# Performance work log

Hardware: AMD Instinct MI355X
Metric: run time of the kernel (lower is better)

Reference implementation:

```python
import jax, jax.numpy as jnp
import numpy as np

B, S, D, H = 2, 2048, 1024, 16
DH = D // H
EPS = 1e-5
NEG = -1e9


def layer_norm(x, scale, bias):
    mu = jnp.mean(x, axis=-1, keepdims=True)
    var = jnp.mean((x - mu) ** 2, axis=-1, keepdims=True)
    return (x - mu) * jax.lax.rsqrt(var + EPS) * scale + bias


def setup_inputs() -> dict:
    key = jax.random.key(0)
    ks = jax.random.split(key, 8)
    scale = 1.0 / np.sqrt(D)
    x = jax.random.normal(ks[0], (B, S, D), dtype=jnp.float32)
    padding_mask = jnp.ones((B, S), dtype=bool)
    # per-head QKV projections stacked over heads: (H, D, DH)
    Wq = jax.random.normal(ks[1], (H, D, DH), dtype=jnp.float32) * scale
    Wk = jax.random.normal(ks[2], (H, D, DH), dtype=jnp.float32) * scale
    Wv = jax.random.normal(ks[3], (H, D, DH), dtype=jnp.float32) * scale
    ln1_s = jnp.ones((D,), jnp.float32); ln1_b = jnp.zeros((D,), jnp.float32)
    ln2_s = jnp.ones((D,), jnp.float32); ln2_b = jnp.zeros((D,), jnp.float32)
    W1 = jax.random.normal(ks[4], (D, D), dtype=jnp.float32) * scale
    b1 = jnp.zeros((D,), jnp.float32)
    W2 = jax.random.normal(ks[5], (D, D), dtype=jnp.float32) * scale
    b2 = jnp.zeros((D,), jnp.float32)
    return dict(x=x, padding_mask=padding_mask, Wq=Wq, Wk=Wk, Wv=Wv,
                ln1_s=ln1_s, ln1_b=ln1_b, ln2_s=ln2_s, ln2_b=ln2_b,
                W1=W1, b1=b1, W2=W2, b2=b2)


def reference(x, padding_mask, Wq, Wk, Wv, ln1_s, ln1_b, ln2_s, ln2_b, W1, b1, W2, b2):
    # pre-norm attention with residual (dropout = identity at eval)
    h = layer_norm(x, ln1_s, ln1_b)
    q = jnp.einsum('bsd,hde->bhse', h, Wq)
    k = jnp.einsum('bsd,hde->bhse', h, Wk)
    v = jnp.einsum('bsd,hde->bhse', h, Wv)
    scores = jnp.einsum('bhse,bhte->bhst', q, k) / jnp.sqrt(jnp.float32(DH))
    causal = jnp.tril(jnp.ones((S, S), dtype=bool))           # (S,S)
    mask = padding_mask[:, None, None, :] & causal[None, None]  # (B,1,S,S)
    scores = jnp.where(mask, scores, NEG)
    p = jax.nn.softmax(scores, axis=-1)
    z = jnp.einsum('bhst,bhte->bshe', p, v).reshape(x.shape[0], x.shape[1], D)
    x = x + z
    # pre-norm FFN with residual
    h2 = layer_norm(x, ln2_s, ln2_b)
    ff = jax.nn.relu(h2 @ W1 + b1) @ W2 + b2
    return x + ff
```

## Files before the change

kernel.cpp:

```cpp
#include <hip/hip_runtime.h>
#include <hip/hip_bf16.h>
#include <stdint.h>

#define NB 2
#define NS 2048
#define ND 1024
#define NH 16
#define NDH 64
#define NT (NB*NS)

using f32x4  = __attribute__((ext_vector_type(4))) float;
using bf16x8 = __attribute__((ext_vector_type(8))) short;

typedef __attribute__((address_space(1))) unsigned int as1_uint;
typedef __attribute__((address_space(3))) unsigned int as3_uint;

#if __has_builtin(__builtin_amdgcn_exp2f)
#define EXP2 __builtin_amdgcn_exp2f
#else
#define EXP2 exp2f
#endif

__device__ __forceinline__ void llds16(void* l, const void* g) {
    __builtin_amdgcn_global_load_lds((as1_uint*)g, (as3_uint*)l, 16, 0, 0);
}

__device__ __forceinline__ f32x4 mfma16(bf16x8 a, bf16x8 b, f32x4 c) {
    return __builtin_amdgcn_mfma_f32_16x16x32_bf16(a, b, c, 0, 0, 0);
}

__device__ __forceinline__ unsigned short f2bf(float f) {
    union { __hip_bfloat16 h; unsigned short u; } cv;
    cv.h = __float2bfloat16(f);
    return cv.u;
}

__global__ void k_prep_ln(const float* __restrict__ Wq, const float* __restrict__ Wk,
                          const float* __restrict__ Wv, const float* __restrict__ W1,
                          const float* __restrict__ W2, unsigned short* __restrict__ WcatT,
                          unsigned short* __restrict__ W1T, unsigned short* __restrict__ W2T,
                          const float* __restrict__ x, const float* __restrict__ sc,
                          const float* __restrict__ bi, unsigned short* __restrict__ hout) {
    __shared__ float tile[64][65];
    __shared__ float ssum[4], ssq[4];
    int tid = threadIdx.x;
    int bid = blockIdx.x;
    if (bid < 768) {
        const float SCALEQ = 0.125f * 1.44269504088896f;
        int kt = bid & 15; bid >>= 4;
        int h  = bid & 15; bid >>= 4;
        int mat = bid;
        const float* W = (mat == 0) ? Wq : (mat == 1) ? Wk : Wv;
#pragma unroll
        for (int i = 0; i < 16; ++i) {
            int idx = tid + i * 256;
            int r = idx >> 6, e = idx & 63;
            tile[r][e] = W[(size_t)h * ND * NDH + (size_t)(kt * 64 + r) * NDH + e];
        }
        __syncthreads();
#pragma unroll
        for (int i = 0; i < 16; ++i) {
            int idx = tid + i * 256;
            int e = idx >> 6, r = idx & 63;
            float v = tile[r][e];
            if (mat == 0) v *= SCALEQ;
            WcatT[(size_t)(mat * 1024 + h * 64 + e) * ND + kt * 64 + r] = f2bf(v);
        }
    } else if (bid < 1280) {
        const float* W = (bid < 1024) ? W1 : W2;
        unsigned short* WT = (bid < 1024) ? W1T : W2T;
        int lb = (bid - 768) & 255;
        int ntile = lb & 15;
        int ktile = lb >> 4;
#pragma unroll
        for (int i = 0; i < 16; ++i) {
            int idx = tid + i * 256;
            int r = idx >> 6, c = idx & 63;
            tile[r][c] = W[(size_t)(ktile * 64 + r) * ND + ntile * 64 + c];
        }
        __syncthreads();
#pragma unroll
        for (int i = 0; i < 16; ++i) {
            int idx = tid + i * 256;
            int c = idx >> 6, r = idx & 63;
            WT[(size_t)(ntile * 64 + c) * ND + ktile * 64 + r] = f2bf(tile[r][c]);
        }
    } else {
        int row = bid - 1280;
        const float* xr = x + (size_t)row * ND;
        float4 v = reinterpret_cast<const float4*>(xr)[tid];
        float sum = v.x + v.y + v.z + v.w;
        float sq  = v.x * v.x + v.y * v.y + v.z * v.z + v.w * v.w;
#pragma unroll
        for (int off = 1; off < 64; off <<= 1) {
            sum += __shfl_xor(sum, off);
            sq  += __shfl_xor(sq, off);
        }
        int wave = tid >> 6;
        if ((tid & 63) == 0) { ssum[wave] = sum; ssq[wave] = sq; }
        __syncthreads();
        sum = ssum[0] + ssum[1] + ssum[2] + ssum[3];
        sq  = ssq[0] + ssq[1] + ssq[2] + ssq[3];
        float mu  = sum * (1.0f / ND);
        float var = sq * (1.0f / ND) - mu * mu;
        float rstd = rsqrtf(var + 1e-5f);
        float4 s4 = reinterpret_cast<const float4*>(sc)[tid];
        float4 b4 = reinterpret_cast<const float4*>(bi)[tid];
        ushort4 o;
        o.x = f2bf((v.x - mu) * rstd * s4.x + b4.x);
        o.y = f2bf((v.y - mu) * rstd * s4.y + b4.y);
        o.z = f2bf((v.z - mu) * rstd * s4.z + b4.z);
        o.w = f2bf((v.w - mu) * rstd * s4.w + b4.w);
        reinterpret_cast<ushort4*>(hout + (size_t)row * ND)[tid] = o;
    }
}

__global__ void k_ln(const float* __restrict__ x, const float* __restrict__ sc,
                     const float* __restrict__ bi, unsigned short* __restrict__ out) {
    int row = blockIdx.x;
    int tid = threadIdx.x;
    const float* xr = x + (size_t)row * ND;
    float4 v = reinterpret_cast<const float4*>(xr)[tid];
    float sum = v.x + v.y + v.z + v.w;
    float sq  = v.x * v.x + v.y * v.y + v.z * v.z + v.w * v.w;
#pragma unroll
    for (int off = 1; off < 64; off <<= 1) {
        sum += __shfl_xor(sum, off);
        sq  += __shfl_xor(sq, off);
    }
    __shared__ float ssum[4], ssq[4];
    int wave = tid >> 6;
    if ((tid & 63) == 0) { ssum[wave] = sum; ssq[wave] = sq; }
    __syncthreads();
    sum = ssum[0] + ssum[1] + ssum[2] + ssum[3];
    sq  = ssq[0] + ssq[1] + ssq[2] + ssq[3];
    float mu  = sum * (1.0f / ND);
    float var = sq * (1.0f / ND) - mu * mu;
    float rstd = rsqrtf(var + 1e-5f);
    float4 s4 = reinterpret_cast<const float4*>(sc)[tid];
    float4 b4 = reinterpret_cast<const float4*>(bi)[tid];
    ushort4 o;
    o.x = f2bf((v.x - mu) * rstd * s4.x + b4.x);
    o.y = f2bf((v.y - mu) * rstd * s4.y + b4.y);
    o.z = f2bf((v.z - mu) * rstd * s4.z + b4.z);
    o.w = f2bf((v.w - mu) * rstd * s4.w + b4.w);
    reinterpret_cast<ushort4*>(out + (size_t)row * ND)[tid] = o;
}

template<bool BIAS, bool RELU, bool RES>
__device__ __forceinline__
void gemm_core(const unsigned short* __restrict__ A, const unsigned short* __restrict__ Bt,
               const float* __restrict__ bias, const float* __restrict__ res,
               void* __restrict__ Cv, int N, int K, int wg) {
    __shared__ __align__(16) unsigned short As[2][64 * 64];
    __shared__ __align__(16) unsigned short Bs[2][128 * 64];
    int tid = threadIdx.x;
    int lane = tid & 63, wave = tid >> 6;
    int wm = wave >> 1, wn = wave & 1;
    int l16 = lane & 15, lg = lane >> 4;
    int ntiles = N >> 7;
    int mt = wg / ntiles;
    int nt = wg % ntiles;

    int srow = tid >> 3;
    int sch  = tid & 7;
    int scs  = sch ^ (srow & 7);
    int KT = K >> 6;

    const unsigned short* Asrc = A  + (size_t)(mt * 64 + srow) * K + scs * 8;
    const unsigned short* Bsrc = Bt + (size_t)(nt * 128 + srow) * K + scs * 8;

    f32x4 acc[2][4];
#pragma unroll
    for (int i = 0; i < 2; ++i)
#pragma unroll
        for (int j = 0; j < 4; ++j) acc[i][j] = (f32x4){0.f, 0.f, 0.f, 0.f};

    auto STAGE = [&](int kt, int bufi) {
        const unsigned short* a = Asrc + kt * 64;
        const unsigned short* b = Bsrc + kt * 64;
        char* ad = (char*)As[bufi] + wave * 1024;
        char* bd = (char*)Bs[bufi] + wave * 1024;
        llds16(ad,         a);
        llds16(ad + 4096,  a + (size_t)32 * K);
        llds16(bd,         b);
        llds16(bd + 4096,  b + (size_t)32 * K);
        llds16(bd + 8192,  b + (size_t)64 * K);
        llds16(bd + 12288, b + (size_t)96 * K);
    };

    auto COMPUTE = [&](int cb) {
        bf16x8 af[2][2], bfb[4][2];
#pragma unroll
        for (int mi = 0; mi < 2; ++mi)
#pragma unroll
            for (int kc = 0; kc < 2; ++kc) {
                int row = wm * 32 + mi * 16 + l16;
                int ch = (kc * 4 + lg) ^ (row & 7);
                af[mi][kc] = *reinterpret_cast<const bf16x8*>((const char*)As[cb] + row * 128 + ch * 16);
            }
#pragma unroll
        for (int ni = 0; ni < 4; ++ni)
#pragma unroll
            for (int kc = 0; kc < 2; ++kc) {
                int row = wn * 64 + ni * 16 + l16;
                int ch = (kc * 4 + lg) ^ (row & 7);
                bfb[ni][kc] = *reinterpret_cast<const bf16x8*>((const char*)Bs[cb] + row * 128 + ch * 16);
            }
#pragma unroll
        for (int mi = 0; mi < 2; ++mi)
#pragma unroll
            for (int ni = 0; ni < 4; ++ni) {
                acc[mi][ni] = mfma16(af[mi][0], bfb[ni][0], acc[mi][ni]);
                acc[mi][ni] = mfma16(af[mi][1], bfb[ni][1], acc[mi][ni]);
            }
    };

    STAGE(0, 0);
    for (int kt = 0; kt < KT; kt += 2) {
        STAGE(kt + 1, 1);
        asm volatile("s_waitcnt vmcnt(6)" ::: "memory");
        __builtin_amdgcn_s_barrier();
        COMPUTE(0);
        __builtin_amdgcn_s_barrier();
        if (kt + 2 < KT) {
            STAGE(kt + 2, 0);
            asm volatile("s_waitcnt vmcnt(6)" ::: "memory");
        } else {
            asm volatile("s_waitcnt vmcnt(0)" ::: "memory");
        }
        __builtin_amdgcn_s_barrier();
        COMPUTE(1);
        __builtin_amdgcn_s_barrier();
    }

#pragma unroll
    for (int mi = 0; mi < 2; ++mi)
#pragma unroll
        for (int ni = 0; ni < 4; ++ni) {
            int col = nt * 128 + wn * 64 + ni * 16 + l16;
            float bv = BIAS ? bias[col] : 0.f;
#pragma unroll
            for (int r = 0; r < 4; ++r) {
                int row = mt * 64 + wm * 32 + mi * 16 + lg * 4 + r;
                float v = acc[mi][ni][r] + bv;
                if (RELU) v = fmaxf(v, 0.f);
                size_t idx = (size_t)row * N + col;
                if (RES) ((float*)Cv)[idx] = v + res[idx];
                else ((unsigned short*)Cv)[idx] = f2bf(v);
            }
        }
}

template<bool BIAS, bool RELU, bool RES>
__device__ __forceinline__
void gemm_core128(const unsigned short* __restrict__ A, const unsigned short* __restrict__ Bt,
                  const float* __restrict__ bias, const float* __restrict__ res,
                  void* __restrict__ Cv, int N, int K, int wg) {
    __shared__ __align__(16) unsigned short As[2][128 * 64];
    __shared__ __align__(16) unsigned short Bs[2][128 * 64];
    int tid = threadIdx.x;
    int lane = tid & 63, wave = tid >> 6;
    int wm = wave >> 1, wn = wave & 1;
    int l16 = lane & 15, lg = lane >> 4;
    int ntiles = N >> 7;
    int mt = wg / ntiles;
    int nt = wg % ntiles;

    int srow = tid >> 3;
    int sch  = tid & 7;
    int scs  = sch ^ (srow & 7);
    int KT = K >> 6;

    const unsigned short* Asrc = A  + (size_t)(mt * 128 + srow) * K + scs * 8;
    const unsigned short* Bsrc = Bt + (size_t)(nt * 128 + srow) * K + scs * 8;

    f32x4 acc[4][4];
#pragma unroll
    for (int i = 0; i < 4; ++i)
#pragma unroll
        for (int j = 0; j < 4; ++j) acc[i][j] = (f32x4){0.f, 0.f, 0.f, 0.f};

    auto STAGE = [&](int kt, int bufi) {
        const unsigned short* a = Asrc + kt * 64;
        const unsigned short* b = Bsrc + kt * 64;
        char* ad = (char*)As[bufi] + wave * 1024;
        char* bd = (char*)Bs[bufi] + wave * 1024;
        llds16(ad,         a);
        llds16(ad + 4096,  a + (size_t)32 * K);
        llds16(ad + 8192,  a + (size_t)64 * K);
        llds16(ad + 12288, a + (size_t)96 * K);
        llds16(bd,         b);
        llds16(bd + 4096,  b + (size_t)32 * K);
        llds16(bd + 8192,  b + (size_t)64 * K);
        llds16(bd + 12288, b + (size_t)96 * K);
    };

    auto COMPUTE = [&](int cb) {
        bf16x8 af[4][2], bfb[4][2];
#pragma unroll
        for (int mi = 0; mi < 4; ++mi)
#pragma unroll
            for (int kc = 0; kc < 2; ++kc) {
                int row = wm * 64 + mi * 16 + l16;
                int ch = (kc * 4 + lg) ^ (row & 7);
                af[mi][kc] = *reinterpret_cast<const bf16x8*>((const char*)As[cb] + row * 128 + ch * 16);
            }
#pragma unroll
        for (int ni = 0; ni < 4; ++ni)
#pragma unroll
            for (int kc = 0; kc < 2; ++kc) {
                int row = wn * 64 + ni * 16 + l16;
                int ch = (kc * 4 + lg) ^ (row & 7);
                bfb[ni][kc] = *reinterpret_cast<const bf16x8*>((const char*)Bs[cb] + row * 128 + ch * 16);
            }
#pragma unroll
        for (int mi = 0; mi < 4; ++mi)
#pragma unroll
            for (int ni = 0; ni < 4; ++ni) {
                acc[mi][ni] = mfma16(af[mi][0], bfb[ni][0], acc[mi][ni]);
                acc[mi][ni] = mfma16(af[mi][1], bfb[ni][1], acc[mi][ni]);
            }
    };

    STAGE(0, 0);
    for (int kt = 0; kt < KT; kt += 2) {
        STAGE(kt + 1, 1);
        asm volatile("s_waitcnt vmcnt(8)" ::: "memory");
        __builtin_amdgcn_s_barrier();
        COMPUTE(0);
        __builtin_amdgcn_s_barrier();
        if (kt + 2 < KT) {
            STAGE(kt + 2, 0);
            asm volatile("s_waitcnt vmcnt(8)" ::: "memory");
        } else {
            asm volatile("s_waitcnt vmcnt(0)" ::: "memory");
        }
        __builtin_amdgcn_s_barrier();
        COMPUTE(1);
        __builtin_amdgcn_s_barrier();
    }

#pragma unroll
    for (int mi = 0; mi < 4; ++mi)
#pragma unroll
        for (int ni = 0; ni < 4; ++ni) {
            int col = nt * 128 + wn * 64 + ni * 16 + l16;
            float bv = BIAS ? bias[col] : 0.f;
#pragma unroll
            for (int r = 0; r < 4; ++r) {
                int row = mt * 128 + wm * 64 + mi * 16 + lg * 4 + r;
                float v = acc[mi][ni][r] + bv;
                if (RELU) v = fmaxf(v, 0.f);
                size_t idx = (size_t)row * N + col;
                if (RES) ((float*)Cv)[idx] = v + res[idx];
                else ((unsigned short*)Cv)[idx] = f2bf(v);
            }
        }
}

template<bool BIAS, bool RELU, bool RES>
__global__ __launch_bounds__(256)
void k_gemm(const unsigned short* __restrict__ A, const unsigned short* __restrict__ Bt,
            const float* __restrict__ bias, const float* __restrict__ res,
            void* __restrict__ Cv, int N, int K) {
    int wg = (blockIdx.x & 7) * (gridDim.x >> 3) + (blockIdx.x >> 3);
    gemm_core<BIAS, RELU, RES>(A, Bt, bias, res, Cv, N, K, wg);
}

__global__ __launch_bounds__(256)
void k_gemm_dual(const unsigned short* __restrict__ A0, const unsigned short* __restrict__ Bt0,
                 void* __restrict__ C0, int N0,
                 const unsigned short* __restrict__ A1, const unsigned short* __restrict__ Bt1,
                 void* __restrict__ C1, int N1, int K, int split) {
    int bid = blockIdx.x;
    if (bid < split) {
        int wg = (bid & 7) * (split >> 3) + (bid >> 3);
        gemm_core128<false, false, false>(A0, Bt0, nullptr, nullptr, C0, N0, K, wg);
    } else {
        int lb = bid - split;
        int nblk = gridDim.x - split;
        int wg = (lb & 7) * (nblk >> 3) + (lb >> 3);
        gemm_core128<false, false, false>(A1, Bt1, nullptr, nullptr, C1, N1, K, wg);
    }
}

__global__ __launch_bounds__(256)
void k_attn(const unsigned short* __restrict__ qk, const unsigned short* __restrict__ VT,
            const float* __restrict__ x, float* __restrict__ x2) {
    constexpr int ldq = 2 * ND;
    int bid = blockIdx.x;
    int bh = bid & 31;
    int s  = (bid >> 5) & 7;
    int g  = bid >> 8;
    int qt = g ? s : 15 - s;
    int h = bh & 15, b = bh >> 4;
    int tid = threadIdx.x;
    int lane = tid & 63, wave = tid >> 6;
    int l16 = lane & 15, lg = lane >> 4;

    const unsigned short* Qp = qk + (size_t)b * NS * ldq + h * NDH;
    const unsigned short* Kp = Qp + ND;
    const unsigned short* Vp = VT + (size_t)(h * NDH) * NT + b * NS;

    __shared__ __align__(16) unsigned short Ks[2][64 * 64];
    __shared__ __align__(16) unsigned short Vs[2][64 * 64];
    __shared__ __align__(16) unsigned short Ps[8][16 * 64];

    int srow = tid >> 3;
    int sch  = tid & 7;
    int scs  = sch ^ (srow & 7);

    int nt = 2 * qt + 2;
    int qw = qt * 128 + wave * 32;

    const unsigned short* Kn = Kp + (size_t)srow * ldq + scs * 8;
    const unsigned short* Vn = Vp + (size_t)srow * NT + scs * 8;

    bf16x8 qfA[2], qfB[2];
#pragma unroll
    for (int kc = 0; kc < 2; ++kc) {
        qfA[kc] = *reinterpret_cast<const bf16x8*>(Qp + (size_t)(qw + l16) * ldq + kc * 32 + lg * 8);
        qfB[kc] = *reinterpret_cast<const bf16x8*>(Qp + (size_t)(qw + 16 + l16) * ldq + kc * 32 + lg * 8);
    }

    bf16x8 vone;
#pragma unroll
    for (int i = 0; i < 8; ++i) vone[i] = (short)0x3F80;

    f32x4 oA[4], oB[4];
#pragma unroll
    for (int i = 0; i < 4; ++i) { oA[i] = (f32x4){0.f,0.f,0.f,0.f}; oB[i] = (f32x4){0.f,0.f,0.f,0.f}; }
    f32x4 lA = (f32x4){0.f,0.f,0.f,0.f}, lB = (f32x4){0.f,0.f,0.f,0.f};

    char* pbA = (char*)&Ps[wave * 2 + 0][0] + l16 * 128;
    char* pbB = (char*)&Ps[wave * 2 + 1][0] + l16 * 128;
    int psw = l16 & 7;

    llds16((char*)Ks[0] + wave * 1024,        Kn);
    llds16((char*)Ks[0] + wave * 1024 + 4096, Kn + (size_t)32 * ldq);
    llds16((char*)Vs[0] + wave * 1024,        Vn);
    llds16((char*)Vs[0] + wave * 1024 + 4096, Vn + (size_t)32 * NT);
    Kn += (size_t)64 * ldq;
    Vn += 64;

    auto BODY = [&](int t, int cur) {
        if (t + 1 < nt) {
            char* kd = (char*)Ks[cur ^ 1] + wave * 1024;
            char* vd = (char*)Vs[cur ^ 1] + wave * 1024;
            llds16(kd,        Kn);
            llds16(kd + 4096, Kn + (size_t)32 * ldq);
            llds16(vd,        Vn);
            llds16(vd + 4096, Vn + (size_t)32 * NT);
            Kn += (size_t)64 * ldq;
            Vn += 64;
            asm volatile("s_waitcnt vmcnt(4)" ::: "memory");
        } else {
            asm volatile("s_waitcnt vmcnt(0)" ::: "memory");
        }
        __builtin_amdgcn_s_barrier();

        f32x4 stA[4], stB[4];
#pragma unroll
        for (int mtt = 0; mtt < 4; ++mtt) { stA[mtt] = (f32x4){0.f,0.f,0.f,0.f}; stB[mtt] = (f32x4){0.f,0.f,0.f,0.f}; }
        __builtin_amdgcn_s_setprio(1);
#pragma unroll
        for (int kc = 0; kc < 2; ++kc)
#pragma unroll
            for (int mtt = 0; mtt < 4; ++mtt) {
                int row = mtt * 16 + l16;
                int ch = (kc * 4 + lg) ^ (row & 7);
                bf16x8 kf = *reinterpret_cast<const bf16x8*>((const char*)Ks[cur] + row * 128 + ch * 16);
                stA[mtt] = mfma16(kf, qfA[kc], stA[mtt]);
                stB[mtt] = mfma16(kf, qfB[kc], stB[mtt]);
            }
        __builtin_amdgcn_s_setprio(0);

        if (64 * t + 63 > qw) {
            int qA = qw + l16, qB = qw + 16 + l16;
#pragma unroll
            for (int mtt = 0; mtt < 4; ++mtt)
#pragma unroll
                for (int r = 0; r < 4; ++r) {
                    int key = t * 64 + mtt * 16 + lg * 4 + r;
                    stA[mtt][r] = (key <= qA) ? stA[mtt][r] : -1.0e30f;
                    stB[mtt][r] = (key <= qB) ? stB[mtt][r] : -1.0e30f;
                }
        }
#pragma unroll
        for (int mtt = 0; mtt < 4; ++mtt) {
            int b0 = mtt * 32 + lg * 8;
            int sb = ((((b0 >> 4) ^ psw) << 4) | (b0 & 15));
            uint2 uA, uB;
            uA.x = (unsigned)f2bf(EXP2(stA[mtt][0])) | ((unsigned)f2bf(EXP2(stA[mtt][1])) << 16);
            uA.y = (unsigned)f2bf(EXP2(stA[mtt][2])) | ((unsigned)f2bf(EXP2(stA[mtt][3])) << 16);
            uB.x = (unsigned)f2bf(EXP2(stB[mtt][0])) | ((unsigned)f2bf(EXP2(stB[mtt][1])) << 16);
            uB.y = (unsigned)f2bf(EXP2(stB[mtt][2])) | ((unsigned)f2bf(EXP2(stB[mtt][3])) << 16);
            *reinterpret_cast<uint2*>(pbA + sb) = uA;
            *reinterpret_cast<uint2*>(pbB + sb) = uB;
        }

        asm volatile("s_waitcnt lgkmcnt(0)" ::: "memory");

        __builtin_amdgcn_s_setprio(1);
#pragma unroll
        for (int kc = 0; kc < 2; ++kc) {
            bf16x8 paA = *reinterpret_cast<const bf16x8*>(pbA + (((kc * 4 + lg) ^ psw) << 4));
            bf16x8 paB = *reinterpret_cast<const bf16x8*>(pbB + (((kc * 4 + lg) ^ psw) << 4));
            lA = mfma16(paA, vone, lA);
            lB = mfma16(paB, vone, lB);
#pragma unroll
            for (int ntt = 0; ntt < 4; ++ntt) {
                int vrow = ntt * 16 + l16;
                bf16x8 vb = *reinterpret_cast<const bf16x8*>(
                    (const char*)Vs[cur] + vrow * 128 + ((((kc * 4 + lg) ^ (vrow & 7)) << 4)));
                oA[ntt] = mfma16(paA, vb, oA[ntt]);
                oB[ntt] = mfma16(paB, vb, oB[ntt]);
            }
        }
        __builtin_amdgcn_s_setprio(0);
        __builtin_amdgcn_s_barrier();
    };

    for (int t = 0; t < nt; t += 2) {
        BODY(t, 0);
        BODY(t + 1, 1);
    }

#pragma unroll
    for (int r = 0; r < 4; ++r) {
        float livA = 1.0f / lA[r];
        float livB = 1.0f / lB[r];
        int tknA = b * NS + qw + lg * 4 + r;
        int tknB = tknA + 16;
        size_t baseA = (size_t)tknA * ND + h * NDH;
        size_t baseB = (size_t)tknB * ND + h * NDH;
#pragma unroll
        for (int ntt = 0; ntt < 4; ++ntt) {
            size_t iA = baseA + ntt * 16 + l16;
            size_t iB = baseB + ntt * 16 + l16;
            x2[iA] = x[iA] + oA[ntt][r] * livA;
            x2[iB] = x[iB] + oB[ntt][r] * livB;
        }
    }
}

extern "C" void kernel_launch(void* const* d_in, const int* in_sizes, int n_in,
                              void* d_out, int out_size, void* d_ws, size_t ws_size,
                              hipStream_t stream) {
    const float* x    = (const float*)d_in[0];
    const float* Wq   = (const float*)d_in[2];
    const float* Wk   = (const float*)d_in[3];
    const float* Wv   = (const float*)d_in[4];
    const float* ln1s = (const float*)d_in[5];
    const float* ln1b = (const float*)d_in[6];
    const float* ln2s = (const float*)d_in[7];
    const float* ln2b = (const float*)d_in[8];
    const float* W1   = (const float*)d_in[9];
    const float* b1   = (const float*)d_in[10];
    const float* W2   = (const float*)d_in[11];
    const float* b2   = (const float*)d_in[12];
    float* out = (float*)d_out;

    char* ws = (char*)d_ws;
    unsigned short* WcatT = (unsigned short*)(ws);
    unsigned short* W1T   = (unsigned short*)(ws + 6291456);
    unsigned short* W2T   = (unsigned short*)(ws + 8388608);
    unsigned short* hbuf  = (unsigned short*)(ws + 10485760);
    unsigned short* qkbuf = (unsigned short*)(ws + 18874368);
    unsigned short* vtbuf = (unsigned short*)(ws + 35651584);
    float*          x2    = (float*)(ws + 44040192);
    unsigned short* ubuf  = qkbuf;

    k_prep_ln<<<1280 + NT, 256, 0, stream>>>(Wq, Wk, Wv, W1, W2, WcatT, W1T, W2T,
                                             x, ln1s, ln1b, hbuf);
    k_gemm_dual<<<512 + 256, 256, 0, stream>>>(
        hbuf, WcatT, qkbuf, 2048,
        WcatT + (size_t)2048 * 1024, hbuf, vtbuf, NT, 1024, 512);
    k_attn<<<512, 256, 0, stream>>>(qkbuf, vtbuf, x, x2);
    k_ln<<<NT, 256, 0, stream>>>(x2, ln2s, ln2b, hbuf);
    k_gemm<true, true, false><<<(NT / 64) * (1024 / 128), 256, 0, stream>>>(
        hbuf, W1T, b1, nullptr, ubuf, 1024, 1024);
    k_gemm<true, false, true><<<(NT / 64) * (1024 / 128), 256, 0, stream>>>(
        ubuf, W2T, b2, x2, out, 1024, 1024);
}
```

Baseline: 134.4 us.

## Split attention into 64-query blocks with 2-wave workgroups and balanced scheduling

The attention kernel now gives each workgroup 64 query rows across 2 waves instead of 128 rows across 4 waves. That doubles the grid to 1024 blocks and reorders them in four groups so long and short causal rows interleave for load balance. Each wave now issues 8 async loads per K/V tile instead of 4, and the causal mask is applied only on the diagonal tile. The change is meant to improve occupancy and the tail balance of the causal triangle. The cost is less K/V reuse per loaded tile, so each K/V tile is fetched twice as many times overall.

```diff
diff --git a/kernel.cpp b/kernel.cpp
--- a/kernel.cpp
+++ b/kernel.cpp
@@ -385,15 +385,16 @@
     }
 }
 
-__global__ __launch_bounds__(256)
+__global__ __launch_bounds__(128)
 void k_attn(const unsigned short* __restrict__ qk, const unsigned short* __restrict__ VT,
             const float* __restrict__ x, float* __restrict__ x2) {
     constexpr int ldq = 2 * ND;
     int bid = blockIdx.x;
-    int bh = bid & 31;
-    int s  = (bid >> 5) & 7;
+    int c  = bid & 255;
     int g  = bid >> 8;
-    int qt = g ? s : 15 - s;
+    int s  = c >> 5;
+    int bh = c & 31;
+    int qb = (g == 0) ? 31 - s : (g == 1) ? 16 + s : (g == 2) ? 15 - s : s;
     int h = bh & 15, b = bh >> 4;
     int tid = threadIdx.x;
     int lane = tid & 63, wave = tid >> 6;
@@ -405,14 +406,14 @@
 
     __shared__ __align__(16) unsigned short Ks[2][64 * 64];
     __shared__ __align__(16) unsigned short Vs[2][64 * 64];
-    __shared__ __align__(16) unsigned short Ps[8][16 * 64];
+    __shared__ __align__(16) unsigned short Ps[4][16 * 64];
 
     int srow = tid >> 3;
     int sch  = tid & 7;
     int scs  = sch ^ (srow & 7);
 
-    int nt = 2 * qt + 2;
-    int qw = qt * 128 + wave * 32;
+    int nt = qb + 1;
+    int qw = qb * 64 + wave * 32;
 
     const unsigned short* Kn = Kp + (size_t)srow * ldq + scs * 8;
     const unsigned short* Vn = Vp + (size_t)srow * NT + scs * 8;
@@ -437,10 +438,15 @@
     char* pbB = (char*)&Ps[wave * 2 + 1][0] + l16 * 128;
     int psw = l16 & 7;
 
-    llds16((char*)Ks[0] + wave * 1024,        Kn);
-    llds16((char*)Ks[0] + wave * 1024 + 4096, Kn + (size_t)32 * ldq);
-    llds16((char*)Vs[0] + wave * 1024,        Vn);
-    llds16((char*)Vs[0] + wave * 1024 + 4096, Vn + (size_t)32 * NT);
+    {
+        char* kd = (char*)Ks[0] + wave * 1024;
+        char* vd = (char*)Vs[0] + wave * 1024;
+#pragma unroll
+        for (int i = 0; i < 4; ++i) {
+            llds16(kd + i * 2048, Kn + (size_t)(16 * i) * ldq);
+            llds16(vd + i * 2048, Vn + (size_t)(16 * i) * NT);
+        }
+    }
     Kn += (size_t)64 * ldq;
     Vn += 64;
 
@@ -448,13 +454,14 @@
         if (t + 1 < nt) {
             char* kd = (char*)Ks[cur ^ 1] + wave * 1024;
             char* vd = (char*)Vs[cur ^ 1] + wave * 1024;
-            llds16(kd,        Kn);
-            llds16(kd + 4096, Kn + (size_t)32 * ldq);
-            llds16(vd,        Vn);
-            llds16(vd + 4096, Vn + (size_t)32 * NT);
+#pragma unroll
+            for (int i = 0; i < 4; ++i) {
+                llds16(kd + i * 2048, Kn + (size_t)(16 * i) * ldq);
+                llds16(vd + i * 2048, Vn + (size_t)(16 * i) * NT);
+            }
             Kn += (size_t)64 * ldq;
             Vn += 64;
-            asm volatile("s_waitcnt vmcnt(4)" ::: "memory");
+            asm volatile("s_waitcnt vmcnt(8)" ::: "memory");
         } else {
             asm volatile("s_waitcnt vmcnt(0)" ::: "memory");
         }
@@ -476,7 +483,7 @@
             }
         __builtin_amdgcn_s_setprio(0);
 
-        if (64 * t + 63 > qw) {
+        if (t == qb) {
             int qA = qw + l16, qB = qw + 16 + l16;
 #pragma unroll
             for (int mtt = 0; mtt < 4; ++mtt)
@@ -524,7 +531,7 @@
 
     for (int t = 0; t < nt; t += 2) {
         BODY(t, 0);
-        BODY(t + 1, 1);
+        if (t + 1 < nt) BODY(t + 1, 1);
     }
 
 #pragma unroll
@@ -577,7 +584,7 @@
     k_gemm_dual<<<512 + 256, 256, 0, stream>>>(
         hbuf, WcatT, qkbuf, 2048,
         WcatT + (size_t)2048 * 1024, hbuf, vtbuf, NT, 1024, 512);
-    k_attn<<<512, 256, 0, stream>>>(qkbuf, vtbuf, x, x2);
+    k_attn<<<NB * NH * 32, 128, 0, stream>>>(qkbuf, vtbuf, x, x2);
     k_ln<<<NT, 256, 0, stream>>>(x2, ln2s, ln2b, hbuf);
     k_gemm<true, true, false><<<(NT / 64) * (1024 / 128), 256, 0, stream>>>(
         hbuf, W1T, b1, nullptr, ubuf, 1024, 1024);
```

After: 131.1 us. 2.4% less time.
